# Optimization experiments

Measured on AMD Instinct MI355X. Metric: run time of the kernel, lower is better.

The kernel has to match this reference:

```python
import jax, jax.numpy as jnp
import numpy as np

N, H, W = 128, 192, 192
THING = 81            # cfg.MODEL.SOGNET.THING_NUM_CLASSES
CLS_DIM = 128         # cls_embedding_dim
POS_DIM = 64          # pos_embedding_dim
REL_DIM = CLS_DIM + POS_DIM


def setup_inputs() -> dict:
    key = jax.random.key(0)
    ks = jax.random.split(key, 8)
    mask_logits = jax.random.normal(ks[0], (1, N, H, W), dtype=jnp.float32)
    # valid boxes: x_max > x_min, y_max > y_min (log(w/h) must be finite)
    xy = jax.random.uniform(ks[1], (N, 2), minval=0.0, maxval=800.0)
    wh = jax.random.uniform(ks[2], (N, 2), minval=16.0, maxval=256.0)
    bbox = jnp.concatenate([xy, xy + wh], axis=1).astype(jnp.float32)
    cls_idx = jax.random.randint(ks[3], (N,), 1, THING)  # values in [1, 80]
    # params (kaiming-normal-ish scale)
    W_U = jax.random.normal(ks[4], (THING - 1, CLS_DIM), jnp.float32) * (2.0 / (THING - 1)) ** 0.5
    W_V = jax.random.normal(ks[5], (THING - 1, CLS_DIM), jnp.float32) * (2.0 / (THING - 1)) ** 0.5
    W_pos = jax.random.normal(ks[6], (4, POS_DIM), jnp.float32) * (2.0 / 4.0) ** 0.5
    W_P = jax.random.normal(ks[7], (REL_DIM, 1), jnp.float32) * (2.0 / REL_DIM) ** 0.5
    return {"mask_logits": mask_logits, "bbox": bbox, "W_U": W_U, "W_V": W_V,
            "W_pos": W_pos, "W_P": W_P, "cls_idx": cls_idx}


def _position_matrix(bbox):
    x_min, y_min, x_max, y_max = bbox[:, 0], bbox[:, 1], bbox[:, 2], bbox[:, 3]
    w = x_max - x_min
    h = y_max - y_min
    x_ctr = (x_min + x_max) / 2.0
    y_ctr = (y_min + y_max) / 2.0
    dx = -(x_ctr[:, None] - x_ctr[None, :]) / w[:, None]          # [N, N]
    dy = -(y_ctr[:, None] - y_ctr[None, :]) / h[:, None]
    dw = jnp.log(w[None, :] / w[:, None])                          # log(w_j / w_i)
    dh = jnp.log(h[None, :] / h[:, None])
    return jnp.stack([dx, dy, dw, dh], axis=2)                     # [N, N, 4]


def reference(mask_logits, bbox, W_U, W_V, W_pos, W_P, cls_idx):
    # --- class relation: outer product of two relu'd class embeddings ---
    one_hot = jax.nn.one_hot(cls_idx - 1, THING - 1, dtype=mask_logits.dtype)  # [N, 80]
    feat1 = jax.nn.relu(one_hot @ W_U)                             # [N, CLS_DIM]
    feat2 = jax.nn.relu(one_hot @ W_V)
    cls_rel = feat1[:, None, :] * feat2[None, :, :]                # [N, N, CLS_DIM]
    # --- position relation: 1x1 conv == linear over last dim ---
    pos_rel = jax.nn.relu(jnp.einsum('ijk,kd->ijd', _position_matrix(bbox), W_pos))  # [N, N, POS_DIM]
    # --- relation score ---
    relation_feat = jnp.concatenate([cls_rel, pos_rel], axis=2)    # [N, N, REL_DIM]
    overlap_score = jax.nn.sigmoid(jnp.einsum('ijk,k->ij', relation_feat, W_P[:, 0]))  # [N, N]
    relation_score = jax.nn.relu(overlap_score - overlap_score.T)  # [N, N]
    # --- relation-weighted mask aggregation ---
    # naive: sum_m (ml*mp)[b,n] * mp[b,m] * score[n,m]  -> factor the m-reduction as a GEMM
    mask_prob = jax.nn.sigmoid(mask_logits)                        # [1, N, H, W]
    weighted = jnp.einsum('nm,bmhw->bnhw', relation_score, mask_prob)
    overlap_part = mask_logits * mask_prob * weighted              # [1, N, H, W]
    return mask_logits - overlap_part
```

## Files before the change

### kernel.cpp

```cpp
#include <hip/hip_runtime.h>

#define HW    36864
#define PXT   144
#define RST   136
#define PST   136

typedef unsigned short u16;
typedef unsigned int   u32;
typedef __attribute__((ext_vector_type(8))) short bf16x8;
typedef __attribute__((ext_vector_type(4))) float f32x4;

__device__ __forceinline__ float bf2f(u32 u) {
    union { u32 i; float f; } c; c.i = u << 16; return c.f;
}
__device__ __forceinline__ u16 f2bf(float f) {
    union { float f; u32 i; } c; c.f = f;
    u32 r = (c.i + 0x7fffu + ((c.i >> 16) & 1u)) >> 16;
    return (u16)r;
}
__device__ __forceinline__ u32 pack2(float a, float b) {
    return (u32)f2bf(a) | ((u32)f2bf(b) << 16);
}
__device__ __forceinline__ float sigf(float x) { return 1.0f / (1.0f + __expf(-x)); }

__device__ __forceinline__ bool is_bf16_blk(const void* ml, int tid) {
    int pred = 0;
    if (tid < 128) {
        u16 v = ((const u16*)ml)[tid];
        u32 e = (v >> 7) & 0xffu;
        pred = ((v & 0x7fffu) == 0 || (e >= 90u && e <= 140u)) ? 1 : 0;
    }
    int cnt = __syncthreads_count(pred);
    return cnt >= 100;
}

__global__ __launch_bounds__(256) void k_rel(
    const void* __restrict__ ml,   const void* __restrict__ bbox,
    const void* __restrict__ WU,   const void* __restrict__ WV,
    const void* __restrict__ Wpos, const void* __restrict__ WP,
    const int* __restrict__ cls,   u16* __restrict__ relN)
{
    const int tid = threadIdx.x;
    const bool bf = is_bf16_blk(ml, tid);
    const int n = blockIdx.x;

    __shared__ float u_s[128], v_s[128], wpos_s[256], wpp_s[64], bbn_s[4];
    __shared__ float d1_s[80], d2_s[80];

    const int cn = cls[n] - 1;
    if (bf) {
        if (tid < 128) {
            float wp = bf2f(((const u16*)WP)[tid]);
            u_s[tid] = fmaxf(bf2f(((const u16*)WU)[cn * 128 + tid]), 0.f) * wp;
            v_s[tid] = fmaxf(bf2f(((const u16*)WV)[cn * 128 + tid]), 0.f) * wp;
        }
        wpos_s[tid] = bf2f(((const u16*)Wpos)[tid]);
        if (tid < 64) wpp_s[tid] = bf2f(((const u16*)WP)[128 + tid]);
        if (tid < 4)  bbn_s[tid] = bf2f(((const u16*)bbox)[n * 4 + tid]);
    } else {
        if (tid < 128) {
            float wp = ((const float*)WP)[tid];
            u_s[tid] = fmaxf(((const float*)WU)[cn * 128 + tid], 0.f) * wp;
            v_s[tid] = fmaxf(((const float*)WV)[cn * 128 + tid], 0.f) * wp;
        }
        wpos_s[tid] = ((const float*)Wpos)[tid];
        if (tid < 64) wpp_s[tid] = ((const float*)WP)[128 + tid];
        if (tid < 4)  bbn_s[tid] = ((const float*)bbox)[n * 4 + tid];
    }
    __syncthreads();

    {
        const int wv_ = tid >> 6, lane = tid & 63;
        const float ua = u_s[lane], ub = u_s[64 + lane];
        const float va = v_s[lane], vb = v_s[64 + lane];
        for (int a = wv_; a < 80; a += 4) {
            float x0, x1, y0, y1;
            if (bf) {
                x0 = bf2f(((const u16*)WV)[a * 128 + lane]);
                x1 = bf2f(((const u16*)WV)[a * 128 + 64 + lane]);
                y0 = bf2f(((const u16*)WU)[a * 128 + lane]);
                y1 = bf2f(((const u16*)WU)[a * 128 + 64 + lane]);
            } else {
                x0 = ((const float*)WV)[a * 128 + lane];
                x1 = ((const float*)WV)[a * 128 + 64 + lane];
                y0 = ((const float*)WU)[a * 128 + lane];
                y1 = ((const float*)WU)[a * 128 + 64 + lane];
            }
            float p1 = ua * fmaxf(x0, 0.f) + ub * fmaxf(x1, 0.f);
            float p2 = va * fmaxf(y0, 0.f) + vb * fmaxf(y1, 0.f);
            #pragma unroll
            for (int o = 32; o; o >>= 1) {
                p1 += __shfl_xor(p1, o);
                p2 += __shfl_xor(p2, o);
            }
            if (lane == 0) { d1_s[a] = p1; d2_s[a] = p2; }
        }
    }
    __syncthreads();

    if (tid >= 128) return;
    const int m = tid;
    const int cm = cls[m] - 1;
    float s1 = d1_s[cm];
    float s2 = d2_s[cm];

    const float xmn = bbn_s[0], ymn = bbn_s[1], xMn = bbn_s[2], yMn = bbn_s[3];
    const float wn = xMn - xmn, hn = yMn - ymn;
    const float xcn = 0.5f * (xmn + xMn), ycn = 0.5f * (ymn + yMn);
    float xmm, ymm, xMm, yMm;
    if (bf) {
        xmm = bf2f(((const u16*)bbox)[m * 4 + 0]); ymm = bf2f(((const u16*)bbox)[m * 4 + 1]);
        xMm = bf2f(((const u16*)bbox)[m * 4 + 2]); yMm = bf2f(((const u16*)bbox)[m * 4 + 3]);
    } else {
        xmm = ((const float*)bbox)[m * 4 + 0]; ymm = ((const float*)bbox)[m * 4 + 1];
        xMm = ((const float*)bbox)[m * 4 + 2]; yMm = ((const float*)bbox)[m * 4 + 3];
    }
    const float wm = xMm - xmm, hm = yMm - ymm;
    const float xcm = 0.5f * (xmm + xMm), ycm = 0.5f * (ymm + yMm);

    const float p0 = -(xcn - xcm) / wn, p1 = -(ycn - ycm) / hn;
    const float p2 = __logf(wm / wn),   p3 = __logf(hm / hn);
    const float q0 = -(xcm - xcn) / wm, q1 = -(ycm - ycn) / hm;
    const float q2 = __logf(wn / wm),   q3 = __logf(hn / hm);

    #pragma unroll 8
    for (int d = 0; d < 64; ++d) {
        float w0 = wpos_s[d], w1 = wpos_s[64 + d], w2 = wpos_s[128 + d], w3 = wpos_s[192 + d];
        float wp = wpp_s[d];
        float t1 = p0 * w0 + p1 * w1 + p2 * w2 + p3 * w3;
        float t2 = q0 * w0 + q1 * w1 + q2 * w2 + q3 * w3;
        s1 += fmaxf(t1, 0.f) * wp;
        s2 += fmaxf(t2, 0.f) * wp;
    }

    float r = fmaxf(sigf(s1) - sigf(s2), 0.f);
    relN[n * 128 + m] = f2bf(r);
}

__global__ __launch_bounds__(512) void k_main(
    const void* __restrict__ mlv, const u16* __restrict__ relN,
    void* __restrict__ outv)
{
    const int tid = threadIdx.x;
    const bool bf = is_bf16_blk(mlv, tid);

    __shared__ u16 rel_s[128 * RST];
    __shared__ u16 prob_t[PXT * PST];

    const int px0  = blockIdx.x * PXT;
    const int lane = tid & 63;
    const int col  = lane & 15;
    const int quad = lane >> 4;
    const int n0   = (tid >> 6) * 16;

    for (int idx = tid; idx < 2048; idx += 512) {
        int r = idx >> 4, c = idx & 15;
        uint4 v = ((const uint4*)relN)[idx];
        *(uint4*)(rel_s + r * RST + c * 8) = v;
    }

    for (int u = tid; u < PXT * 16; u += 512) {
        int px = u % PXT, kg = u / PXT;
        size_t gbase = (size_t)(kg * 8) * HW + px0 + px;
        float f[8];
        if (bf) {
            #pragma unroll
            for (int j = 0; j < 8; ++j)
                f[j] = bf2f((u32)((const u16*)mlv)[gbase + (size_t)j * HW]);
        } else {
            #pragma unroll
            for (int j = 0; j < 8; ++j)
                f[j] = ((const float*)mlv)[gbase + (size_t)j * HW];
        }
        uint4 o;
        o.x = pack2(sigf(f[0]), sigf(f[1]));
        o.y = pack2(sigf(f[2]), sigf(f[3]));
        o.z = pack2(sigf(f[4]), sigf(f[5]));
        o.w = pack2(sigf(f[6]), sigf(f[7]));
        *(uint4*)(prob_t + px * PST + kg * 8) = o;
    }
    __syncthreads();

    f32x4 acc[9];
    #pragma unroll
    for (int t = 0; t < 9; ++t) acc[t] = (f32x4){0.f, 0.f, 0.f, 0.f};

    #pragma unroll
    for (int ks = 0; ks < 4; ++ks) {
        const int k0 = ks * 32 + quad * 8;
        bf16x8 a = *(const bf16x8*)(rel_s + (n0 + col) * RST + k0);
        #pragma unroll
        for (int t = 0; t < 9; ++t) {
            bf16x8 b = *(const bf16x8*)(prob_t + (t * 16 + col) * PST + k0);
            acc[t] = __builtin_amdgcn_mfma_f32_16x16x32_bf16(a, b, acc[t], 0, 0, 0);
        }
    }

    #pragma unroll
    for (int t = 0; t < 9; ++t) {
        const int px = px0 + t * 16 + col;
        #pragma unroll
        for (int r = 0; r < 4; ++r) {
            size_t off = (size_t)(n0 + quad * 4 + r) * HW + px;
            if (bf) {
                float mlvv = bf2f((u32)((const u16*)mlv)[off]);
                float pr = sigf(mlvv);
                ((u16*)outv)[off] = f2bf(mlvv - mlvv * pr * acc[t][r]);
            } else {
                float mlvv = ((const float*)mlv)[off];
                float pr = sigf(mlvv);
                ((float*)outv)[off] = mlvv - mlvv * pr * acc[t][r];
            }
        }
    }
}

extern "C" void kernel_launch(void* const* d_in, const int* in_sizes, int n_in,
                              void* d_out, int out_size, void* d_ws, size_t ws_size,
                              hipStream_t stream) {
    const void* ml   = d_in[0];
    const void* bbox = d_in[1];
    const void* WU   = d_in[2];
    const void* WV   = d_in[3];
    const void* Wpos = d_in[4];
    const void* WP   = d_in[5];
    const int*  cls  = (const int*)d_in[6];

    u16* relN = (u16*)d_ws;

    k_rel<<<dim3(128), dim3(256), 0, stream>>>(ml, bbox, WU, WV, Wpos, WP, cls, relN);
    k_main<<<dim3(256), dim3(512), 0, stream>>>(ml, relN, d_out);
}
```

Measured before the change: 111.7 us.

## Split prob tile load into two K halves to overlap loads with MFMA

```diff
diff --git a/kernel.cpp b/kernel.cpp
--- a/kernel.cpp
+++ b/kernel.cpp
@@ -159,34 +159,83 @@
         *(uint4*)(rel_s + r * RST + c * 8) = v;
     }
 
-    for (int u = tid; u < PXT * 16; u += 512) {
-        int px = u % PXT, kg = u / PXT;
-        size_t gbase = (size_t)(kg * 8) * HW + px0 + px;
-        float f[8];
-        if (bf) {
-            #pragma unroll
-            for (int j = 0; j < 8; ++j)
-                f[j] = bf2f((u32)((const u16*)mlv)[gbase + (size_t)j * HW]);
-        } else {
-            #pragma unroll
-            for (int j = 0; j < 8; ++j)
-                f[j] = ((const float*)mlv)[gbase + (size_t)j * HW];
-        }
-        uint4 o;
-        o.x = pack2(sigf(f[0]), sigf(f[1]));
-        o.y = pack2(sigf(f[2]), sigf(f[3]));
-        o.z = pack2(sigf(f[4]), sigf(f[5]));
-        o.w = pack2(sigf(f[6]), sigf(f[7]));
-        *(uint4*)(prob_t + px * PST + kg * 8) = o;
-    }
-    __syncthreads();
+    #pragma unroll
+    for (int i = 0; i < 3; ++i) {
+        int u = tid + i * 512;
+        if (u < PXT * 8) {
+            int px = u % PXT, kg = u / PXT;
+            size_t gbase = (size_t)(kg * 8) * HW + px0 + px;
+            float f[8];
+            if (bf) {
+                #pragma unroll
+                for (int j = 0; j < 8; ++j)
+                    f[j] = bf2f((u32)((const u16*)mlv)[gbase + (size_t)j * HW]);
+            } else {
+                #pragma unroll
+                for (int j = 0; j < 8; ++j)
+                    f[j] = ((const float*)mlv)[gbase + (size_t)j * HW];
+            }
+            uint4 o;
+            o.x = pack2(sigf(f[0]), sigf(f[1]));
+            o.y = pack2(sigf(f[2]), sigf(f[3]));
+            o.z = pack2(sigf(f[4]), sigf(f[5]));
+            o.w = pack2(sigf(f[6]), sigf(f[7]));
+            *(uint4*)(prob_t + px * PST + kg * 8) = o;
+        }
+    }
+    __syncthreads();
+
+    float hf[3][8];
+    #pragma unroll
+    for (int i = 0; i < 3; ++i) {
+        int u = tid + i * 512;
+        if (u < PXT * 8) {
+            int px = u % PXT, kg = 8 + u / PXT;
+            size_t gbase = (size_t)(kg * 8) * HW + px0 + px;
+            if (bf) {
+                #pragma unroll
+                for (int j = 0; j < 8; ++j)
+                    hf[i][j] = bf2f((u32)((const u16*)mlv)[gbase + (size_t)j * HW]);
+            } else {
+                #pragma unroll
+                for (int j = 0; j < 8; ++j)
+                    hf[i][j] = ((const float*)mlv)[gbase + (size_t)j * HW];
+            }
+        }
+    }
 
     f32x4 acc[9];
     #pragma unroll
     for (int t = 0; t < 9; ++t) acc[t] = (f32x4){0.f, 0.f, 0.f, 0.f};
 
     #pragma unroll
-    for (int ks = 0; ks < 4; ++ks) {
+    for (int ks = 0; ks < 2; ++ks) {
+        const int k0 = ks * 32 + quad * 8;
+        bf16x8 a = *(const bf16x8*)(rel_s + (n0 + col) * RST + k0);
+        #pragma unroll
+        for (int t = 0; t < 9; ++t) {
+            bf16x8 b = *(const bf16x8*)(prob_t + (t * 16 + col) * PST + k0);
+            acc[t] = __builtin_amdgcn_mfma_f32_16x16x32_bf16(a, b, acc[t], 0, 0, 0);
+        }
+    }
+
+    #pragma unroll
+    for (int i = 0; i < 3; ++i) {
+        int u = tid + i * 512;
+        if (u < PXT * 8) {
+            int px = u % PXT, kg = 8 + u / PXT;
+            uint4 o;
+            o.x = pack2(sigf(hf[i][0]), sigf(hf[i][1]));
+            o.y = pack2(sigf(hf[i][2]), sigf(hf[i][3]));
+            o.z = pack2(sigf(hf[i][4]), sigf(hf[i][5]));
+            o.w = pack2(sigf(hf[i][6]), sigf(hf[i][7]));
+            *(uint4*)(prob_t + px * PST + kg * 8) = o;
+        }
+    }
+    __syncthreads();
+
+    #pragma unroll
+    for (int ks = 2; ks < 4; ++ks) {
         const int k0 = ks * 32 + quad * 8;
         bf16x8 a = *(const bf16x8*)(rel_s + (n0 + col) * RST + k0);
         #pragma unroll
```

After: 113.9 us. Within noise of the previous version (+1.9%).
